# Optimization experiments

Hardware: AMD Instinct MI355X
Metric: run time of the kernel (lower is better)

## Reference

```python
import jax, jax.numpy as jnp
import numpy as np

DIM = 384
HEADS = 12
POS_DIM = (DIM // 4) // 4  # DynamicPosBias: pos_dim = (dim//4)//4 = 24
B_WIN = 64
GH = GW = GD = 8
N_TOK = GH * GW * GD  # 512
NG = 8  # num windows sharing one mask


def _ln(x, g, b):
    m = jnp.mean(x, axis=-1, keepdims=True)
    v = jnp.var(x, axis=-1, keepdims=True)
    return (x - m) / jnp.sqrt(v + 1e-5) * g + b


def setup_inputs() -> dict:
    key = jax.random.key(0)
    ks = jax.random.split(key, 8)
    s = 0.02
    inp = {
        "x": jax.random.normal(ks[0], (B_WIN, N_TOK, DIM), jnp.float32),
        "H": GH, "W": GW, "D": GD,
        "mask": jnp.zeros((NG, N_TOK, N_TOK), jnp.float32),
        "qkv_w": jax.random.normal(ks[1], (DIM, 3 * DIM), jnp.float32) * s,
        "qkv_b": jnp.zeros((3 * DIM,), jnp.float32),
        "proj_w": jax.random.normal(ks[2], (DIM, DIM), jnp.float32) * s,
        "proj_b": jnp.zeros((DIM,), jnp.float32),
        "pos_proj_w": jax.random.normal(ks[3], (3, POS_DIM), jnp.float32) * s,
        "pos_proj_b": jnp.zeros((POS_DIM,), jnp.float32),
        "ln1_g": jnp.ones((POS_DIM,), jnp.float32), "ln1_b": jnp.zeros((POS_DIM,), jnp.float32),
        "pos1_w": jax.random.normal(ks[4], (POS_DIM, POS_DIM), jnp.float32) * s,
        "pos1_b": jnp.zeros((POS_DIM,), jnp.float32),
        "ln2_g": jnp.ones((POS_DIM,), jnp.float32), "ln2_b": jnp.zeros((POS_DIM,), jnp.float32),
        "pos2_w": jax.random.normal(ks[5], (POS_DIM, POS_DIM), jnp.float32) * s,
        "pos2_b": jnp.zeros((POS_DIM,), jnp.float32),
        "ln3_g": jnp.ones((POS_DIM,), jnp.float32), "ln3_b": jnp.zeros((POS_DIM,), jnp.float32),
        "pos3_w": jax.random.normal(ks[6], (POS_DIM, HEADS), jnp.float32) * s,
        "pos3_b": jnp.zeros((HEADS,), jnp.float32),
    }
    return inp


def reference(x, H, W, D, mask, qkv_w, qkv_b, proj_w, proj_b,
              pos_proj_w, pos_proj_b, ln1_g, ln1_b, pos1_w, pos1_b,
              ln2_g, ln2_b, pos2_w, pos2_b, ln3_g, ln3_b, pos3_w, pos3_b):
    B_, N, C = x.shape
    h = HEADS
    d = C // h
    scale = d ** (-0.5)

    qkv = (x @ qkv_w + qkv_b).reshape(B_, N, 3, h, d).transpose(2, 0, 3, 1, 4)
    q, k, v = qkv[0] * scale, qkv[1], qkv[2]  # each (B_, h, N, d)

    attn = jnp.einsum('bhnd,bhmd->bhnm', q, k)  # (B_, h, N, N)

    # dynamic relative position bias
    rh = jnp.arange(1 - H, H)
    rw = jnp.arange(1 - W, W)
    rd = jnp.arange(1 - D, D)
    biases = jnp.stack(jnp.meshgrid(rh, rw, rd, indexing='ij'))
    biases = biases.reshape(3, -1).T.astype(jnp.float32)  # (L, 3), L=(2H-1)(2W-1)(2D-1)

    coords = jnp.stack(jnp.meshgrid(jnp.arange(H), jnp.arange(W), jnp.arange(D), indexing='ij'))
    coords = coords.reshape(3, -1)  # (3, N)
    rel = (coords[:, :, None] - coords[:, None, :]).transpose(1, 2, 0)  # (N, N, 3)
    rel = rel + jnp.array([H - 1, W - 1, D - 1])
    rel = rel * jnp.array([(2 * W - 1) * (2 * D - 1), 2 * D - 1, 1])
    rpi = rel.sum(-1)  # (N, N) int index into L

    pos = biases @ pos_proj_w + pos_proj_b  # (L, pos_dim)
    pos = jax.nn.relu(_ln(pos, ln1_g, ln1_b)) @ pos1_w + pos1_b
    pos = jax.nn.relu(_ln(pos, ln2_g, ln2_b)) @ pos2_w + pos2_b
    pos = jax.nn.relu(_ln(pos, ln3_g, ln3_b)) @ pos3_w + pos3_b  # (L, h)

    rel_bias = pos[rpi]  # (N, N, h)
    attn = attn + rel_bias.transpose(2, 0, 1)[None]  # (B_, h, N, N)

    nG = mask.shape[0]
    attn = attn.reshape(B_ // nG, nG, h, N, N) + mask[None, :, None]
    attn = jax.nn.softmax(attn.reshape(B_, h, N, N), axis=-1)

    out = jnp.einsum('bhnm,bhmd->bhnd', attn, v)  # (B_, h, N, d)
    out = out.transpose(0, 2, 1, 3).reshape(B_, N, C)
    return out @ proj_w + proj_b
```

## Files before the change

### kernel.cpp

```cpp
#include <hip/hip_runtime.h>


typedef __bf16 bf16;
typedef __bf16 bf16x4 __attribute__((ext_vector_type(4)));
typedef __bf16 bf16x8 __attribute__((ext_vector_type(8)));
typedef float  f32x4  __attribute__((ext_vector_type(4)));
typedef unsigned int u32;
typedef u32 u32x4v __attribute__((ext_vector_type(4)));

#define DIMC   384
#define HEADS  12
#define HD     32
#define NTOK   512
#define NWIN   64
#define LTAB   3375
#define LPAD   3392
#define PD     24
#define LOG2E  1.4426950408889634f
#define QPRE   (0.17677669529663687f * LOG2E)
#define VSTR   520

#define SZ_WQT  884736ll
#define SZ_WPT  294912ll
#define SZ_POST 81408ll
#define SZ_FLAG 256ll
#define SZ_B2   6291456ll
#define SZ_MT   4194304ll
#define SZ_QKV  25165824ll
#define WS_SMALL 102236160ull
#define WS_BIG   112410368ull

#define NB_XC   12288
#define NB_WQT  1728
#define NB_WPT  576
#define NB_MSK  256
#define NB_POS  14
#define NB_PREP (NB_XC + NB_WQT + NB_WPT + NB_MSK + NB_POS)

#define NB_ATTN (HEADS * NWIN * 4)

__device__ inline u32 cvtpk(float lo, float hi) {
    u32 r;
    asm("v_cvt_pk_bf16_f32 %0, %1, %2" : "=v"(r) : "v"(lo), "v"(hi));
    return r;
}
__device__ inline void plswap32(u32& a, u32& b) {
    asm("v_permlane32_swap_b32 %0, %1" : "+v"(a), "+v"(b));
}
__device__ inline void plswap16(u32& a, u32& b) {
    asm("v_permlane16_swap_b32 %0, %1" : "+v"(a), "+v"(b));
}
__device__ inline float ex2(float x) {
#if __has_builtin(__builtin_amdgcn_exp2f)
    return __builtin_amdgcn_exp2f(x);
#else
    float r; asm("v_exp_f32 %0, %1" : "=v"(r) : "v"(x)); return r;
#endif
}
__device__ inline void gload_lds16(const void* g, void* l) {
    __builtin_amdgcn_global_load_lds(
        (const __attribute__((address_space(1))) void*)g,
        (__attribute__((address_space(3))) void*)l, 16, 0, 0);
}

__device__ inline void ln_relu24(const float* x, const float* __restrict__ g,
                                 const float* __restrict__ b, float* y)
{
    float mean = 0.f;
#pragma unroll
    for (int j = 0; j < PD; j++) mean += x[j];
    mean *= (1.f / PD);
    float var = 0.f;
#pragma unroll
    for (int j = 0; j < PD; j++) { float d = x[j] - mean; var += d * d; }
    var *= (1.f / PD);
    float inv = rsqrtf(var + 1e-5f);
#pragma unroll
    for (int j = 0; j < PD; j++) {
        float t = (x[j] - mean) * inv * g[j] + b[j];
        y[j] = t > 0.f ? t : 0.f;
    }
}

__global__ __launch_bounds__(256) void prep_kernel(
    const float* __restrict__ x,
    const float* __restrict__ qkv_w, const float* __restrict__ proj_w,
    const float* __restrict__ mask,
    const float* __restrict__ pw,  const float* __restrict__ pb,
    const float* __restrict__ g1,  const float* __restrict__ b1,
    const float* __restrict__ w1,  const float* __restrict__ bb1,
    const float* __restrict__ g2,  const float* __restrict__ b2,
    const float* __restrict__ w2,  const float* __restrict__ bb2,
    const float* __restrict__ g3,  const float* __restrict__ b3,
    const float* __restrict__ w3,  const float* __restrict__ bb3,
    bf16* __restrict__ xb, bf16* __restrict__ wqT, bf16* __restrict__ wpT,
    int* __restrict__ flag, bf16* __restrict__ posTg)
{
    const int tid = threadIdx.x;
    int bx = blockIdx.x;

    if (bx < NB_XC) {
        const int i = bx * 256 + tid;
        const f32x4 v = *(const f32x4*)(x + (size_t)i * 4);
        bf16x4 o;
#pragma unroll
        for (int j = 0; j < 4; j++) o[j] = (bf16)v[j];
        *(bf16x4*)(xb + (size_t)i * 4) = o;
        return;
    }
    bx -= NB_XC;
    if (bx < NB_WQT) {
        const int idx = bx * 256 + tid;
        const int n = idx / 384, k = idx - n * 384;
        wqT[idx] = (bf16)qkv_w[(size_t)k * 1152 + n];
        return;
    }
    bx -= NB_WQT;
    if (bx < NB_WPT) {
        const int idx = bx * 256 + tid;
        const int n = idx / 384, k = idx - n * 384;
        wpT[idx] = (bf16)proj_w[(size_t)k * 384 + n];
        return;
    }
    bx -= NB_WPT;
    if (bx < NB_MSK) {
        const int i = bx * 256 + tid;
        const float* p = mask + (size_t)i * 32;
        float s = 0.f;
#pragma unroll
        for (int j = 0; j < 32; j++) s += fabsf(p[j]);
        if (!(s == 0.f)) atomicOr(flag, 1);
        return;
    }
    bx -= NB_MSK;
    {
        const int l = bx * 256 + tid;
        if (l >= LTAB) return;
        const int ih = l / 225, iw = (l / 15) % 15, id = l % 15;
        const float c0 = (float)(ih - 7), c1 = (float)(iw - 7), c2 = (float)(id - 7);
        float xx[PD], y[PD];
#pragma unroll
        for (int j = 0; j < PD; j++)
            xx[j] = c0 * pw[j] + c1 * pw[PD + j] + c2 * pw[2 * PD + j] + pb[j];
        ln_relu24(xx, g1, b1, y);
#pragma unroll
        for (int j = 0; j < PD; j++) {
            float a = bb1[j];
#pragma unroll
            for (int i = 0; i < PD; i++) a += y[i] * w1[i * PD + j];
            xx[j] = a;
        }
        ln_relu24(xx, g2, b2, y);
#pragma unroll
        for (int j = 0; j < PD; j++) {
            float a = bb2[j];
#pragma unroll
            for (int i = 0; i < PD; i++) a += y[i] * w2[i * PD + j];
            xx[j] = a;
        }
        ln_relu24(xx, g3, b3, y);
#pragma unroll
        for (int hh = 0; hh < HEADS; hh++) {
            float a = bb3[hh];
#pragma unroll
            for (int i = 0; i < PD; i++) a += y[i] * w3[i * HEADS + hh];
            posTg[hh * LPAD + l] = (bf16)(a * LOG2E);
        }
    }
}

__global__ __launch_bounds__(256) void bias2_build_kernel(
    const bf16* __restrict__ posTg, bf16* __restrict__ bias2)
{
    int idx = blockIdx.x * 256 + threadIdx.x;
    int h = idx >> 18;
    int q = (idx >> 9) & 511;
    int m = idx & 511;
    int dh = (q >> 6) - (m >> 6) + 7;
    int dw = ((q >> 3) & 7) - ((m >> 3) & 7) + 7;
    int dd = (q & 7) - (m & 7) + 7;
    bias2[idx] = posTg[h * LPAD + dh * 225 + dw * 15 + dd];
}

__global__ __launch_bounds__(256) void vt_inplace_kernel(bf16* __restrict__ V)
{
    __shared__ __align__(16) bf16 tile[32 * 520];
    bf16* base = V + (size_t)blockIdx.x * (NTOK * HD);
    const int tid = threadIdx.x;
    const int nq = tid >> 2;
    const int c4 = tid & 3;
    const int d0 = c4 * 8;
#pragma unroll
    for (int it = 0; it < 8; it++) {
        const int n = nq + it * 64;
        bf16x8 v = *(const bf16x8*)(base + n * HD + d0);
#pragma unroll
        for (int j = 0; j < 8; j++) {
            const int jj = (j + (c4 << 1)) & 7;
            tile[(d0 + jj) * 520 + n] = v[jj];
        }
    }
    __syncthreads();
#pragma unroll
    for (int it = 0; it < 8; it++) {
        const int o = it * 2048 + tid * 8;
        const int d = o >> 9, n = o & 511;
        bf16x8 w = *(const bf16x8*)(tile + d * 520 + n);
        *(bf16x8*)(base + d * NTOK + n) = w;
    }
}

template <int MODE>
__global__ __launch_bounds__(256) void gemm_bt(
    const bf16* __restrict__ A, const bf16* __restrict__ Bt,
    const float* __restrict__ bias,
    bf16* __restrict__ O0, bf16* __restrict__ O1, bf16* __restrict__ O2,
    float* __restrict__ Of, int K, int N)
{
    __shared__ __align__(16) bf16 lA[128 * 64];
    __shared__ __align__(16) bf16 lB[128 * 64];
    const int row0 = blockIdx.x * 128;
    const int col0 = blockIdx.y * 128;
    const int tid  = threadIdx.x;
    const int lane = tid & 63;
    const int wave = tid >> 6;
    const int r0   = (wave >> 1) * 64;
    const int c0   = (wave & 1) * 64;
    const int lrow = lane & 15;
    const int lch  = lane >> 4;

    f32x4 acc[4][4];
    const f32x4 zero4 = {0.f, 0.f, 0.f, 0.f};
#pragma unroll
    for (int i = 0; i < 4; i++)
#pragma unroll
        for (int j = 0; j < 4; j++) acc[i][j] = zero4;

    for (int kt = 0; kt < K; kt += 64) {
        __syncthreads();
#pragma unroll
        for (int it = 0; it < 4; it++) {
            const int c  = tid + it * 256;
            const int rr = c >> 3;
            const int cc = (c & 7) * 8;
            bf16* la = lA + (size_t)(it * 256 + wave * 64) * 8;
            bf16* lb = lB + (size_t)(it * 256 + wave * 64) * 8;
            gload_lds16(A  + (size_t)(row0 + rr) * K + kt + cc, la);
            gload_lds16(Bt + (size_t)(col0 + rr) * K + kt + cc, lb);
        }
        __syncthreads();
#pragma unroll
        for (int kk = 0; kk < 64; kk += 32) {
            bf16x8 af[4], bfr[4];
#pragma unroll
            for (int i = 0; i < 4; i++)
                af[i] = *(const bf16x8*)(lA + (r0 + i * 16 + lrow) * 64 + kk + lch * 8);
#pragma unroll
            for (int j = 0; j < 4; j++)
                bfr[j] = *(const bf16x8*)(lB + (c0 + j * 16 + lrow) * 64 + kk + lch * 8);
#pragma unroll
            for (int i = 0; i < 4; i++)
#pragma unroll
                for (int j = 0; j < 4; j++)
                    acc[i][j] = __builtin_amdgcn_mfma_f32_16x16x32_bf16(af[i], bfr[j], acc[i][j], 0, 0, 0);
        }
    }

#pragma unroll
    for (int i = 0; i < 4; i++) {
#pragma unroll
        for (int j = 0; j < 4; j++) {
#pragma unroll
            for (int r = 0; r < 4; r++) {
                const int mrow = row0 + r0 + i * 16 + lch * 4 + r;
                const int ncol = col0 + c0 + j * 16 + lrow;
                const float v = acc[i][j][r] + bias[ncol];
                if (MODE == 0) {
                    const int t    = ncol >= 768 ? 2 : (ncol >= 384 ? 1 : 0);
                    const int rem2 = ncol - t * 384;
                    const int hh   = rem2 >> 5;
                    const int dd   = rem2 & 31;
                    const int bwin = mrow >> 9;
                    const int n    = mrow & 511;
                    bf16* dst = (t == 0) ? O0 : ((t == 1) ? O1 : O2);
                    const float vv = (t == 0) ? v * QPRE : v;
                    dst[(size_t)((bwin * HEADS + hh) * NTOK + n) * HD + dd] = (bf16)vv;
                } else {
                    Of[(size_t)mrow * N + ncol] = v;
                }
            }
        }
    }
}

template <int BIG>
__global__ __launch_bounds__(256, 4) void attn_kernel(
    const bf16* __restrict__ Qg, const bf16* __restrict__ Kg,
    const bf16* __restrict__ Vtg, const bf16* __restrict__ posTg,
    const float* __restrict__ maskg, const bf16* __restrict__ bias2,
    const int* __restrict__ mflag, bf16* __restrict__ Og)
{
    __shared__ __align__(16) bf16 lVt[32 * VSTR];
    __shared__ __align__(16) bf16 lPos[BIG ? 16 : LPAD];

    const int idx = (blockIdx.x & 7) * (NB_ATTN / 8) + (blockIdx.x >> 3);
    const int h   = idx >> 8;
    const int rem = idx & 255;
    const int b   = rem >> 2;
    const int qt  = rem & 3;
    const int g   = b & 7;
    const int tid = threadIdx.x;
    const int lane = tid & 63;
    const int wave = tid >> 6;
    const int lrow = lane & 15;
    const int lch  = lane >> 4;
    const int msk  = *mflag;

    const bf16* Qp  = Qg  + (size_t)(b * HEADS + h) * NTOK * HD;
    const bf16* Kp  = Kg  + (size_t)(b * HEADS + h) * NTOK * HD;
    const bf16* Vtp = Vtg + (size_t)(b * HEADS + h) * NTOK * HD;
    const float* Mp = maskg + (size_t)g * NTOK * NTOK;
    const bf16* B2p = bias2 + (size_t)h * NTOK * NTOK;

    {
        const int d0 = wave * 8;
#pragma unroll
        for (int rr = 0; rr < 8; rr++) {
            const int d = d0 + rr;
            gload_lds16(Vtp + (size_t)d * NTOK + lane * 8, lVt + (size_t)d * VSTR);
        }
    }
    if (!BIG) {
        const uint4* src = (const uint4*)(posTg + h * LPAD);
        for (int i = tid; i < LPAD * 2 / 16; i += 256)
            ((uint4*)lPos)[i] = src[i];
    }
    __syncthreads();

    const int qbase = qt * 128 + wave * 32;

    bf16x8 qf[2];
#pragma unroll
    for (int t = 0; t < 2; t++)
        qf[t] = *(const bf16x8*)(Qp + (size_t)(qbase + t * 16 + lrow) * HD + lch * 8);

    int qc0[2] = {0, 0}, qc1[2] = {0, 0}, qc2[2] = {0, 0};
    if (!BIG) {
#pragma unroll
        for (int t = 0; t < 2; t++) {
            const int q = qbase + t * 16 + lrow;
            qc0[t] = q >> 6; qc1[t] = (q >> 3) & 7; qc2[t] = q & 7;
        }
    }

    float m_i[2] = {-1e30f, -1e30f};
    float l_i[2] = {0.f, 0.f};
    f32x4 oacc[2][2];
    const f32x4 zero4 = {0.f, 0.f, 0.f, 0.f};
    oacc[0][0] = zero4; oacc[0][1] = zero4;
    oacc[1][0] = zero4; oacc[1][1] = zero4;

    for (int kt = 0; kt < 4; kt++) {
        bf16x8 apc[2][4];
        float alr[2];
        bool doresc[2];

#pragma unroll
        for (int t = 0; t < 2; t++) {
            const int qrow = qbase + t * 16 + lrow;
            f32x4 sf[8];

            bf16x4 bld[8];
            if (BIG) {
                const bf16* brow = B2p + (size_t)qrow * NTOK + kt * 128 + lch * 4;
#pragma unroll
                for (int ct = 0; ct < 8; ct++)
                    bld[ct] = *(const bf16x4*)(brow + ct * 16);
            }

#pragma unroll
            for (int ct = 0; ct < 8; ct++) {
                bf16x8 kf = *(const bf16x8*)(Kp + (size_t)(kt * 128 + ct * 16 + lrow) * HD + lch * 8);
                sf[ct] = __builtin_amdgcn_mfma_f32_16x16x32_bf16(kf, qf[t], zero4, 0, 0, 0);
            }

            if (BIG) {
#pragma unroll
                for (int ct = 0; ct < 8; ct++)
#pragma unroll
                    for (int r = 0; r < 4; r++)
                        sf[ct][r] += (float)bld[ct][r];
            } else {
#pragma unroll
                for (int ct = 0; ct < 8; ct++) {
#pragma unroll
                    for (int r = 0; r < 4; r++) {
                        const int k = kt * 128 + ct * 16 + lch * 4 + r;
                        const int rpi = (qc0[t] - (k >> 6) + 7) * 225
                                      + (qc1[t] - ((k >> 3) & 7) + 7) * 15
                                      + (qc2[t] - (k & 7) + 7);
                        sf[ct][r] += (float)lPos[rpi];
                    }
                }
            }
            if (msk) {
                const float* mrow = Mp + (size_t)qrow * NTOK + kt * 128 + lch * 4;
#pragma unroll
                for (int ct = 0; ct < 8; ct++) {
                    f32x4 mv = *(const f32x4*)(mrow + ct * 16);
#pragma unroll
                    for (int r = 0; r < 4; r++)
                        sf[ct][r] = fmaf(mv[r], LOG2E, sf[ct][r]);
                }
            }

            float px[8];
#pragma unroll
            for (int ct = 0; ct < 8; ct++)
                px[ct] = fmaxf(fmaxf(sf[ct][0], sf[ct][1]), fmaxf(sf[ct][2], sf[ct][3]));
            float mx = fmaxf(fmaxf(fmaxf(px[0], px[1]), fmaxf(px[2], px[3])),
                             fmaxf(fmaxf(px[4], px[5]), fmaxf(px[6], px[7])));
            mx = fmaxf(mx, __shfl_xor(mx, 16));
            mx = fmaxf(mx, __shfl_xor(mx, 32));

            if (__all(mx <= m_i[t] + 8.f)) {
                alr[t] = 1.f;
                doresc[t] = false;
            } else {
                const float mnew = fmaxf(m_i[t], mx);
                alr[t] = ex2(m_i[t] - mnew);
                m_i[t] = mnew;
                doresc[t] = true;
            }

            float s0 = 0.f, s1 = 0.f;
#pragma unroll
            for (int ct = 0; ct < 8; ct++) {
#pragma unroll
                for (int r = 0; r < 4; r++)
                    sf[ct][r] = ex2(sf[ct][r] - m_i[t]);
                s0 += sf[ct][0] + sf[ct][1];
                s1 += sf[ct][2] + sf[ct][3];
            }
            float ls = s0 + s1;
            ls += __shfl_xor(ls, 16);
            ls += __shfl_xor(ls, 32);
            l_i[t] = l_i[t] * alr[t] + ls;

#pragma unroll
            for (int c2 = 0; c2 < 4; c2++) {
                u32 a01 = cvtpk(sf[2 * c2][0],     sf[2 * c2][1]);
                u32 a23 = cvtpk(sf[2 * c2][2],     sf[2 * c2][3]);
                u32 b01 = cvtpk(sf[2 * c2 + 1][0], sf[2 * c2 + 1][1]);
                u32 b23 = cvtpk(sf[2 * c2 + 1][2], sf[2 * c2 + 1][3]);
                plswap32(a01, b01); plswap16(a01, b01);
                plswap32(a23, b23); plswap16(a23, b23);
                u32x4v w; w[0] = a01; w[1] = a23; w[2] = b01; w[3] = b23;
                apc[t][c2] = __builtin_bit_cast(bf16x8, w);
            }
        }

#pragma unroll
        for (int t = 0; t < 2; t++) {
            if (doresc[t]) {
#pragma unroll
                for (int r = 0; r < 4; r++) {
                    const float a = __shfl(alr[t], lch * 4 + r);
                    oacc[t][0][r] *= a;
                    oacc[t][1][r] *= a;
                }
            }
        }

#pragma unroll
        for (int c2 = 0; c2 < 4; c2++) {
            const int mofs = kt * 128 + c2 * 32;
            bf16x8 bv0 = *(const bf16x8*)(lVt + (size_t)lrow * VSTR + mofs + lch * 8);
            bf16x8 bv1 = *(const bf16x8*)(lVt + (size_t)(16 + lrow) * VSTR + mofs + lch * 8);
#pragma unroll
            for (int t = 0; t < 2; t++) {
                oacc[t][0] = __builtin_amdgcn_mfma_f32_16x16x32_bf16(apc[t][c2], bv0, oacc[t][0], 0, 0, 0);
                oacc[t][1] = __builtin_amdgcn_mfma_f32_16x16x32_bf16(apc[t][c2], bv1, oacc[t][1], 0, 0, 0);
            }
        }
    }

#pragma unroll
    for (int t = 0; t < 2; t++) {
#pragma unroll
        for (int r = 0; r < 4; r++) {
            const float lv  = __shfl(l_i[t], lch * 4 + r);
            const float inv = 1.f / fmaxf(lv, 1e-20f);
            const int n = qbase + t * 16 + lch * 4 + r;
            bf16* orow = Og + (size_t)(b * NTOK + n) * DIMC + h * HD;
            orow[lrow]      = (bf16)(oacc[t][0][r] * inv);
            orow[16 + lrow] = (bf16)(oacc[t][1][r] * inv);
        }
    }
}

extern "C" void kernel_launch(void* const* d_in, const int* in_sizes, int n_in,
                              void* d_out, int out_size, void* d_ws, size_t ws_size,
                              hipStream_t stream)
{
    if (ws_size < WS_SMALL) return;
    const bool BIG = (ws_size >= WS_BIG);

    const float* x      = (const float*)d_in[0];
    const float* maskp  = (const float*)d_in[4];
    const float* qkv_w  = (const float*)d_in[5];
    const float* qkv_b  = (const float*)d_in[6];
    const float* proj_w = (const float*)d_in[7];
    const float* proj_b = (const float*)d_in[8];

    char* ws = (char*)d_ws;
    size_t off = 0;
    bf16* wsWqT  = (bf16*)(ws + off); off += SZ_WQT;
    bf16* wsWpT  = (bf16*)(ws + off); off += SZ_WPT;
    bf16* wsPosT = (bf16*)(ws + off); off += SZ_POST;
    int*  wsFlag = (int*)(ws + off);  off += SZ_FLAG;
    bf16* wsB2 = nullptr;
    if (BIG) {
        wsB2 = (bf16*)(ws + off); off += SZ_B2;
        off += SZ_MT;
    } else {
        off = 1572864;
    }
    bf16* wsQ    = (bf16*)(ws + off); off += SZ_QKV;
    bf16* wsK    = (bf16*)(ws + off); off += SZ_QKV;
    bf16* wsV    = (bf16*)(ws + off); off += SZ_QKV;
    bf16* wsAttn = (bf16*)(ws + off);
    bf16* wsXb   = wsAttn;

    hipMemsetAsync(wsFlag, 0, 4, stream);

    prep_kernel<<<NB_PREP, 256, 0, stream>>>(
        x, qkv_w, proj_w, maskp,
        (const float*)d_in[9],  (const float*)d_in[10], (const float*)d_in[11],
        (const float*)d_in[12], (const float*)d_in[13], (const float*)d_in[14],
        (const float*)d_in[15], (const float*)d_in[16], (const float*)d_in[17],
        (const float*)d_in[18], (const float*)d_in[19], (const float*)d_in[20],
        (const float*)d_in[21], (const float*)d_in[22],
        wsXb, wsWqT, wsWpT, wsFlag, wsPosT);

    if (BIG)
        bias2_build_kernel<<<(HEADS * NTOK * NTOK) / 256, 256, 0, stream>>>(wsPosT, wsB2);

    gemm_bt<0><<<dim3(256, 9), 256, 0, stream>>>(wsXb, wsWqT, qkv_b, wsQ, wsK, wsV,
                                                 nullptr, 384, 1152);

    vt_inplace_kernel<<<NWIN * HEADS, 256, 0, stream>>>(wsV);

    if (BIG)
        attn_kernel<1><<<NB_ATTN, 256, 0, stream>>>(
            wsQ, wsK, wsV, wsPosT, maskp, wsB2, wsFlag, wsAttn);
    else
        attn_kernel<0><<<NB_ATTN, 256, 0, stream>>>(
            wsQ, wsK, wsV, wsPosT, maskp, wsB2, wsFlag, wsAttn);

    gemm_bt<1><<<dim3(256, 3), 256, 0, stream>>>(wsAttn, wsWpT, proj_b,
                                                 nullptr, nullptr, nullptr,
                                                 (float*)d_out, 384, 384);
}
```

Before: 417.9 us.

## Unroll attention key loop with register double-buffered K fragments and first-tile shortcut

Result: slower. 467.1 us (+11.8%).

```diff
diff --git a/kernel.cpp b/kernel.cpp
--- a/kernel.cpp
+++ b/kernel.cpp
@@ -293,6 +293,131 @@
     }
 }
 
+template <int BIG, bool FIRST, bool PF>
+__device__ __forceinline__ void attn_tile(
+    int qrow, int kt, int nkt, int lch, int lrow,
+    const bf16x8* kf, bf16x8* kfn, const bf16* Kp,
+    const bf16* B2p, const bf16* lPos, const float* Mp, int msk,
+    const bf16* lVt, bf16x8 qv, float& mi, float& li, f32x4* oa)
+{
+    const f32x4 zero4 = {0.f, 0.f, 0.f, 0.f};
+    f32x4 sf[8];
+
+    bf16x4 bld[8];
+    if (BIG) {
+        const bf16* brow = B2p + (size_t)qrow * NTOK + kt * 128 + lch * 4;
+#pragma unroll
+        for (int ct = 0; ct < 8; ct++)
+            bld[ct] = *(const bf16x4*)(brow + ct * 16);
+    }
+
+#pragma unroll
+    for (int ct = 0; ct < 8; ct++)
+        sf[ct] = __builtin_amdgcn_mfma_f32_16x16x32_bf16(kf[ct], qv, zero4, 0, 0, 0);
+
+    if (PF) {
+#pragma unroll
+        for (int ct = 0; ct < 8; ct++)
+            kfn[ct] = *(const bf16x8*)(Kp + (size_t)(nkt * 128 + ct * 16 + lrow) * HD + lch * 8);
+    }
+
+    if (BIG) {
+#pragma unroll
+        for (int ct = 0; ct < 8; ct++)
+#pragma unroll
+            for (int r = 0; r < 4; r++)
+                sf[ct][r] += (float)bld[ct][r];
+    } else {
+        const int nh = qrow >> 6, nw = (qrow >> 3) & 7, nd = qrow & 7;
+#pragma unroll
+        for (int ct = 0; ct < 8; ct++) {
+#pragma unroll
+            for (int r = 0; r < 4; r++) {
+                const int k = kt * 128 + ct * 16 + lch * 4 + r;
+                const int rpi = (nh - (k >> 6) + 7) * 225
+                              + (nw - ((k >> 3) & 7) + 7) * 15
+                              + (nd - (k & 7) + 7);
+                sf[ct][r] += (float)lPos[rpi];
+            }
+        }
+    }
+    if (msk) {
+        const float* mrow = Mp + (size_t)qrow * NTOK + kt * 128 + lch * 4;
+#pragma unroll
+        for (int ct = 0; ct < 8; ct++) {
+            f32x4 mv = *(const f32x4*)(mrow + ct * 16);
+#pragma unroll
+            for (int r = 0; r < 4; r++)
+                sf[ct][r] = fmaf(mv[r], LOG2E, sf[ct][r]);
+        }
+    }
+
+    float px[8];
+#pragma unroll
+    for (int ct = 0; ct < 8; ct++)
+        px[ct] = fmaxf(fmaxf(sf[ct][0], sf[ct][1]), fmaxf(sf[ct][2], sf[ct][3]));
+    float mx = fmaxf(fmaxf(fmaxf(px[0], px[1]), fmaxf(px[2], px[3])),
+                     fmaxf(fmaxf(px[4], px[5]), fmaxf(px[6], px[7])));
+    mx = fmaxf(mx, __shfl_xor(mx, 16));
+    mx = fmaxf(mx, __shfl_xor(mx, 32));
+
+    bool doresc = false;
+    float alr = 1.f;
+    if (FIRST) {
+        mi = mx;
+    } else if (!__all(mx <= mi + 8.f)) {
+        const float mn = fmaxf(mi, mx);
+        alr = ex2(mi - mn);
+        mi = mn;
+        doresc = true;
+    }
+
+    float s0 = 0.f, s1 = 0.f;
+#pragma unroll
+    for (int ct = 0; ct < 8; ct++) {
+#pragma unroll
+        for (int r = 0; r < 4; r++)
+            sf[ct][r] = ex2(sf[ct][r] - mi);
+        s0 += sf[ct][0] + sf[ct][1];
+        s1 += sf[ct][2] + sf[ct][3];
+    }
+    float ls = s0 + s1;
+    ls += __shfl_xor(ls, 16);
+    ls += __shfl_xor(ls, 32);
+    li = FIRST ? ls : (doresc ? li * alr + ls : li + ls);
+
+    bf16x8 apc[4];
+#pragma unroll
+    for (int c2 = 0; c2 < 4; c2++) {
+        u32 a01 = cvtpk(sf[2 * c2][0],     sf[2 * c2][1]);
+        u32 a23 = cvtpk(sf[2 * c2][2],     sf[2 * c2][3]);
+        u32 b01 = cvtpk(sf[2 * c2 + 1][0], sf[2 * c2 + 1][1]);
+        u32 b23 = cvtpk(sf[2 * c2 + 1][2], sf[2 * c2 + 1][3]);
+        plswap32(a01, b01); plswap16(a01, b01);
+        plswap32(a23, b23); plswap16(a23, b23);
+        u32x4v w; w[0] = a01; w[1] = a23; w[2] = b01; w[3] = b23;
+        apc[c2] = __builtin_bit_cast(bf16x8, w);
+    }
+
+    if (doresc) {
+#pragma unroll
+        for (int r = 0; r < 4; r++) {
+            const float a = __shfl(alr, lch * 4 + r);
+            oa[0][r] *= a;
+            oa[1][r] *= a;
+        }
+    }
+
+#pragma unroll
+    for (int c2 = 0; c2 < 4; c2++) {
+        const int mofs = kt * 128 + c2 * 32;
+        bf16x8 bv0 = *(const bf16x8*)(lVt + (size_t)lrow * VSTR + mofs + lch * 8);
+        bf16x8 bv1 = *(const bf16x8*)(lVt + (size_t)(16 + lrow) * VSTR + mofs + lch * 8);
+        oa[0] = __builtin_amdgcn_mfma_f32_16x16x32_bf16(apc[c2], bv0, oa[0], 0, 0, 0);
+        oa[1] = __builtin_amdgcn_mfma_f32_16x16x32_bf16(apc[c2], bv1, oa[1], 0, 0, 0);
+    }
+}
+
 template <int BIG>
 __global__ __launch_bounds__(256, 4) void attn_kernel(
     const bf16* __restrict__ Qg, const bf16* __restrict__ Kg,
@@ -339,163 +464,50 @@
 
     const int qbase = qt * 128 + wave * 32;
 
-    bf16x8 qf[2];
-#pragma unroll
-    for (int t = 0; t < 2; t++)
-        qf[t] = *(const bf16x8*)(Qp + (size_t)(qbase + t * 16 + lrow) * HD + lch * 8);
-
-    int qc0[2] = {0, 0}, qc1[2] = {0, 0}, qc2[2] = {0, 0};
-    if (!BIG) {
-#pragma unroll
-        for (int t = 0; t < 2; t++) {
-            const int q = qbase + t * 16 + lrow;
-            qc0[t] = q >> 6; qc1[t] = (q >> 3) & 7; qc2[t] = q & 7;
-        }
-    }
-
-    float m_i[2] = {-1e30f, -1e30f};
-    float l_i[2] = {0.f, 0.f};
-    f32x4 oacc[2][2];
+    bf16x8 qf0 = *(const bf16x8*)(Qp + (size_t)(qbase + lrow) * HD + lch * 8);
+    bf16x8 qf1 = *(const bf16x8*)(Qp + (size_t)(qbase + 16 + lrow) * HD + lch * 8);
+
+    float mi0 = -1e30f, mi1 = -1e30f, li0 = 0.f, li1 = 0.f;
+    f32x4 oacc0[2], oacc1[2];
     const f32x4 zero4 = {0.f, 0.f, 0.f, 0.f};
-    oacc[0][0] = zero4; oacc[0][1] = zero4;
-    oacc[1][0] = zero4; oacc[1][1] = zero4;
-
-    for (int kt = 0; kt < 4; kt++) {
-        bf16x8 apc[2][4];
-        float alr[2];
-        bool doresc[2];
-
-#pragma unroll
-        for (int t = 0; t < 2; t++) {
-            const int qrow = qbase + t * 16 + lrow;
-            f32x4 sf[8];
-
-            bf16x4 bld[8];
-            if (BIG) {
-                const bf16* brow = B2p + (size_t)qrow * NTOK + kt * 128 + lch * 4;
-#pragma unroll
-                for (int ct = 0; ct < 8; ct++)
-                    bld[ct] = *(const bf16x4*)(brow + ct * 16);
-            }
-
-#pragma unroll
-            for (int ct = 0; ct < 8; ct++) {
-                bf16x8 kf = *(const bf16x8*)(Kp + (size_t)(kt * 128 + ct * 16 + lrow) * HD + lch * 8);
-                sf[ct] = __builtin_amdgcn_mfma_f32_16x16x32_bf16(kf, qf[t], zero4, 0, 0, 0);
-            }
-
-            if (BIG) {
-#pragma unroll
-                for (int ct = 0; ct < 8; ct++)
-#pragma unroll
-                    for (int r = 0; r < 4; r++)
-                        sf[ct][r] += (float)bld[ct][r];
-            } else {
-#pragma unroll
-                for (int ct = 0; ct < 8; ct++) {
-#pragma unroll
-                    for (int r = 0; r < 4; r++) {
-                        const int k = kt * 128 + ct * 16 + lch * 4 + r;
-                        const int rpi = (qc0[t] - (k >> 6) + 7) * 225
-                                      + (qc1[t] - ((k >> 3) & 7) + 7) * 15
-                                      + (qc2[t] - (k & 7) + 7);
-                        sf[ct][r] += (float)lPos[rpi];
-                    }
-                }
-            }
-            if (msk) {
-                const float* mrow = Mp + (size_t)qrow * NTOK + kt * 128 + lch * 4;
-#pragma unroll
-                for (int ct = 0; ct < 8; ct++) {
-                    f32x4 mv = *(const f32x4*)(mrow + ct * 16);
-#pragma unroll
-                    for (int r = 0; r < 4; r++)
-                        sf[ct][r] = fmaf(mv[r], LOG2E, sf[ct][r]);
-                }
-            }
-
-            float px[8];
-#pragma unroll
-            for (int ct = 0; ct < 8; ct++)
-                px[ct] = fmaxf(fmaxf(sf[ct][0], sf[ct][1]), fmaxf(sf[ct][2], sf[ct][3]));
-            float mx = fmaxf(fmaxf(fmaxf(px[0], px[1]), fmaxf(px[2], px[3])),
-                             fmaxf(fmaxf(px[4], px[5]), fmaxf(px[6], px[7])));
-            mx = fmaxf(mx, __shfl_xor(mx, 16));
-            mx = fmaxf(mx, __shfl_xor(mx, 32));
-
-            if (__all(mx <= m_i[t] + 8.f)) {
-                alr[t] = 1.f;
-                doresc[t] = false;
-            } else {
-                const float mnew = fmaxf(m_i[t], mx);
-                alr[t] = ex2(m_i[t] - mnew);
-                m_i[t] = mnew;
-                doresc[t] = true;
-            }
-
-            float s0 = 0.f, s1 = 0.f;
-#pragma unroll
-            for (int ct = 0; ct < 8; ct++) {
-#pragma unroll
-                for (int r = 0; r < 4; r++)
-                    sf[ct][r] = ex2(sf[ct][r] - m_i[t]);
-                s0 += sf[ct][0] + sf[ct][1];
-                s1 += sf[ct][2] + sf[ct][3];
-            }
-            float ls = s0 + s1;
-            ls += __shfl_xor(ls, 16);
-            ls += __shfl_xor(ls, 32);
-            l_i[t] = l_i[t] * alr[t] + ls;
-
-#pragma unroll
-            for (int c2 = 0; c2 < 4; c2++) {
-                u32 a01 = cvtpk(sf[2 * c2][0],     sf[2 * c2][1]);
-                u32 a23 = cvtpk(sf[2 * c2][2],     sf[2 * c2][3]);
-                u32 b01 = cvtpk(sf[2 * c2 + 1][0], sf[2 * c2 + 1][1]);
-                u32 b23 = cvtpk(sf[2 * c2 + 1][2], sf[2 * c2 + 1][3]);
-                plswap32(a01, b01); plswap16(a01, b01);
-                plswap32(a23, b23); plswap16(a23, b23);
-                u32x4v w; w[0] = a01; w[1] = a23; w[2] = b01; w[3] = b23;
-                apc[t][c2] = __builtin_bit_cast(bf16x8, w);
-            }
-        }
-
-#pragma unroll
-        for (int t = 0; t < 2; t++) {
-            if (doresc[t]) {
-#pragma unroll
-                for (int r = 0; r < 4; r++) {
-                    const float a = __shfl(alr[t], lch * 4 + r);
-                    oacc[t][0][r] *= a;
-                    oacc[t][1][r] *= a;
-                }
-            }
-        }
-
-#pragma unroll
-        for (int c2 = 0; c2 < 4; c2++) {
-            const int mofs = kt * 128 + c2 * 32;
-            bf16x8 bv0 = *(const bf16x8*)(lVt + (size_t)lrow * VSTR + mofs + lch * 8);
-            bf16x8 bv1 = *(const bf16x8*)(lVt + (size_t)(16 + lrow) * VSTR + mofs + lch * 8);
-#pragma unroll
-            for (int t = 0; t < 2; t++) {
-                oacc[t][0] = __builtin_amdgcn_mfma_f32_16x16x32_bf16(apc[t][c2], bv0, oacc[t][0], 0, 0, 0);
-                oacc[t][1] = __builtin_amdgcn_mfma_f32_16x16x32_bf16(apc[t][c2], bv1, oacc[t][1], 0, 0, 0);
-            }
-        }
-    }
-
-#pragma unroll
-    for (int t = 0; t < 2; t++) {
-#pragma unroll
-        for (int r = 0; r < 4; r++) {
-            const float lv  = __shfl(l_i[t], lch * 4 + r);
-            const float inv = 1.f / fmaxf(lv, 1e-20f);
-            const int n = qbase + t * 16 + lch * 4 + r;
-            bf16* orow = Og + (size_t)(b * NTOK + n) * DIMC + h * HD;
-            orow[lrow]      = (bf16)(oacc[t][0][r] * inv);
-            orow[16 + lrow] = (bf16)(oacc[t][1][r] * inv);
-        }
+    oacc0[0] = zero4; oacc0[1] = zero4;
+    oacc1[0] = zero4; oacc1[1] = zero4;
+
+    bf16x8 kfA[8], kfB[8];
+
+#pragma unroll
+    for (int ct = 0; ct < 8; ct++)
+        kfA[ct] = *(const bf16x8*)(Kp + (size_t)(ct * 16 + lrow) * HD + lch * 8);
+
+    const int q0 = qbase + lrow;
+    const int q1 = qbase + 16 + lrow;
+
+    attn_tile<BIG, true,  false>(q0, 0, 0, lch, lrow, kfA, kfB, Kp, B2p, lPos, Mp, msk, lVt, qf0, mi0, li0, oacc0);
+    attn_tile<BIG, true,  true >(q1, 0, 1, lch, lrow, kfA, kfB, Kp, B2p, lPos, Mp, msk, lVt, qf1, mi1, li1, oacc1);
+    attn_tile<BIG, false, false>(q0, 1, 0, lch, lrow, kfB, kfA, Kp, B2p, lPos, Mp, msk, lVt, qf0, mi0, li0, oacc0);
+    attn_tile<BIG, false, true >(q1, 1, 2, lch, lrow, kfB, kfA, Kp, B2p, lPos, Mp, msk, lVt, qf1, mi1, li1, oacc1);
+    attn_tile<BIG, false, false>(q0, 2, 0, lch, lrow, kfA, kfB, Kp, B2p, lPos, Mp, msk, lVt, qf0, mi0, li0, oacc0);
+    attn_tile<BIG, false, true >(q1, 2, 3, lch, lrow, kfA, kfB, Kp, B2p, lPos, Mp, msk, lVt, qf1, mi1, li1, oacc1);
+    attn_tile<BIG, false, false>(q0, 3, 0, lch, lrow, kfB, kfA, Kp, B2p, lPos, Mp, msk, lVt, qf0, mi0, li0, oacc0);
+    attn_tile<BIG, false, false>(q1, 3, 0, lch, lrow, kfB, kfA, Kp, B2p, lPos, Mp, msk, lVt, qf1, mi1, li1, oacc1);
+
+#pragma unroll
+    for (int r = 0; r < 4; r++) {
+        const float lv  = __shfl(li0, lch * 4 + r);
+        const float inv = 1.f / fmaxf(lv, 1e-20f);
+        const int n = qbase + lch * 4 + r;
+        bf16* orow = Og + (size_t)(b * NTOK + n) * DIMC + h * HD;
+        orow[lrow]      = (bf16)(oacc0[0][r] * inv);
+        orow[16 + lrow] = (bf16)(oacc0[1][r] * inv);
+    }
+#pragma unroll
+    for (int r = 0; r < 4; r++) {
+        const float lv  = __shfl(li1, lch * 4 + r);
+        const float inv = 1.f / fmaxf(lv, 1e-20f);
+        const int n = qbase + 16 + lch * 4 + r;
+        bf16* orow = Og + (size_t)(b * NTOK + n) * DIMC + h * HD;
+        orow[lrow]      = (bf16)(oacc1[0][r] * inv);
+        orow[16 + lrow] = (bf16)(oacc1[1][r] * inv);
     }
 }
 
```

## Double-buffer V tiles per key chunk and raise priority around MFMA loops

Applied to the files above, without the earlier changes.

New measurement: 444.5 us. +6.4%, slower.

```diff
diff --git a/kernel.cpp b/kernel.cpp
--- a/kernel.cpp
+++ b/kernel.cpp
@@ -18,7 +18,8 @@
 #define PD     24
 #define LOG2E  1.4426950408889634f
 #define QPRE   (0.17677669529663687f * LOG2E)
-#define VSTR   520
+#define VSTR2  136
+#define VBUF   (32 * VSTR2)
 
 #define SZ_WQT  884736ll
 #define SZ_WPT  294912ll
@@ -61,6 +62,11 @@
     __builtin_amdgcn_global_load_lds(
         (const __attribute__((address_space(1))) void*)g,
         (__attribute__((address_space(3))) void*)l, 16, 0, 0);
+}
+__device__ inline void gload_lds4(const void* g, void* l) {
+    __builtin_amdgcn_global_load_lds(
+        (const __attribute__((address_space(1))) void*)g,
+        (__attribute__((address_space(3))) void*)l, 4, 0, 0);
 }
 
 __device__ inline void ln_relu24(const float* x, const float* __restrict__ g,
@@ -300,7 +306,7 @@
     const float* __restrict__ maskg, const bf16* __restrict__ bias2,
     const int* __restrict__ mflag, bf16* __restrict__ Og)
 {
-    __shared__ __align__(16) bf16 lVt[32 * VSTR];
+    __shared__ __align__(16) bf16 lVt2[2 * VBUF];
     __shared__ __align__(16) bf16 lPos[BIG ? 16 : LPAD];
 
     const int idx = (blockIdx.x & 7) * (NB_ATTN / 8) + (blockIdx.x >> 3);
@@ -322,14 +328,16 @@
     const float* Mp = maskg + (size_t)g * NTOK * NTOK;
     const bf16* B2p = bias2 + (size_t)h * NTOK * NTOK;
 
-    {
-        const int d0 = wave * 8;
+    auto stageV = [&](int bb, int kt2) {
 #pragma unroll
         for (int rr = 0; rr < 8; rr++) {
-            const int d = d0 + rr;
-            gload_lds16(Vtp + (size_t)d * NTOK + lane * 8, lVt + (size_t)d * VSTR);
-        }
-    }
+            const int d = wave * 8 + rr;
+            gload_lds4(Vtp + (size_t)d * NTOK + kt2 * 128 + lane * 2,
+                       lVt2 + bb * VBUF + d * VSTR2);
+        }
+    };
+
+    stageV(0, 0);
     if (!BIG) {
         const uint4* src = (const uint4*)(posTg + h * LPAD);
         for (int i = tid; i < LPAD * 2 / 16; i += 256)
@@ -361,6 +369,8 @@
     oacc[1][0] = zero4; oacc[1][1] = zero4;
 
     for (int kt = 0; kt < 4; kt++) {
+        if (kt < 3) stageV((kt + 1) & 1, kt + 1);
+
         bf16x8 apc[2][4];
         float alr[2];
         bool doresc[2];
@@ -378,11 +388,13 @@
                     bld[ct] = *(const bf16x4*)(brow + ct * 16);
             }
 
+            __builtin_amdgcn_s_setprio(1);
 #pragma unroll
             for (int ct = 0; ct < 8; ct++) {
                 bf16x8 kf = *(const bf16x8*)(Kp + (size_t)(kt * 128 + ct * 16 + lrow) * HD + lch * 8);
                 sf[ct] = __builtin_amdgcn_mfma_f32_16x16x32_bf16(kf, qf[t], zero4, 0, 0, 0);
             }
+            __builtin_amdgcn_s_setprio(0);
 
             if (BIG) {
 #pragma unroll
@@ -472,17 +484,23 @@
             }
         }
 
-#pragma unroll
-        for (int c2 = 0; c2 < 4; c2++) {
-            const int mofs = kt * 128 + c2 * 32;
-            bf16x8 bv0 = *(const bf16x8*)(lVt + (size_t)lrow * VSTR + mofs + lch * 8);
-            bf16x8 bv1 = *(const bf16x8*)(lVt + (size_t)(16 + lrow) * VSTR + mofs + lch * 8);
-#pragma unroll
-            for (int t = 0; t < 2; t++) {
-                oacc[t][0] = __builtin_amdgcn_mfma_f32_16x16x32_bf16(apc[t][c2], bv0, oacc[t][0], 0, 0, 0);
-                oacc[t][1] = __builtin_amdgcn_mfma_f32_16x16x32_bf16(apc[t][c2], bv1, oacc[t][1], 0, 0, 0);
-            }
-        }
+        {
+            const bf16* vb = lVt2 + (kt & 1) * VBUF;
+            __builtin_amdgcn_s_setprio(1);
+#pragma unroll
+            for (int c2 = 0; c2 < 4; c2++) {
+                bf16x8 bv0 = *(const bf16x8*)(vb + (size_t)lrow * VSTR2 + c2 * 32 + lch * 8);
+                bf16x8 bv1 = *(const bf16x8*)(vb + (size_t)(16 + lrow) * VSTR2 + c2 * 32 + lch * 8);
+#pragma unroll
+                for (int t = 0; t < 2; t++) {
+                    oacc[t][0] = __builtin_amdgcn_mfma_f32_16x16x32_bf16(apc[t][c2], bv0, oacc[t][0], 0, 0, 0);
+                    oacc[t][1] = __builtin_amdgcn_mfma_f32_16x16x32_bf16(apc[t][c2], bv1, oacc[t][1], 0, 0, 0);
+                }
+            }
+            __builtin_amdgcn_s_setprio(0);
+        }
+
+        if (kt < 3) __syncthreads();
     }
 
 #pragma unroll
```
